# Kernel tuning notes

Measured on AMD Instinct MI355X. Metric: run time of the kernel, lower is better.

Reference implementation:

```python
import jax, jax.numpy as jnp
import numpy as np

B, S = 1, 1536
D_MODEL, NHEAD, HEAD_DIM = 1024, 16, 64
ROPE, NUM_SEQ = 32, 4
KVC, QC, D_FF = 256, 384, 4096
SPP = S // NUM_SEQ                      # seq per stock = 384
EPS_RMS = 1.1920929e-07                 # torch RMSNorm default eps = finfo(fp32).eps
ATTN_EPS = 1e-5
LAMBDA_INIT = 0.8 - 0.6 * float(np.exp(-0.3 * 0.0))  # depth 0 -> 0.2
SCALING = float(((HEAD_DIM + ROPE) // 2) ** -0.5)


def rmsnorm(x, w, eps=EPS_RMS):
    var = jnp.mean(jnp.square(x), axis=-1, keepdims=True)
    return x * jax.lax.rsqrt(var + eps) * w


def setup_inputs() -> dict:
    key = jax.random.key(0)
    ks = jax.random.split(key, 16)
    sd = 0.02
    inv_freq = 1.0 / (10000.0 ** (np.arange(0, ROPE // 4) / (ROPE // 4)))
    ang = np.arange(1, SPP)[:, None] * inv_freq[None, :]  # [SPP-1, ROPE//4]
    return {
        "x": jax.random.normal(ks[0], (B, S, D_MODEL), jnp.float32),
        "freqs_cos": jnp.asarray(np.cos(ang), jnp.float32),
        "freqs_sin": jnp.asarray(np.sin(ang), jnp.float32),
        "norm1_w": jnp.ones((D_MODEL,), jnp.float32),
        "norm2_w": jnp.ones((D_MODEL,), jnp.float32),
        "kv_down_w": jax.random.normal(ks[1], (KVC + ROPE, D_MODEL), jnp.float32) * sd,
        "q_down_w": jax.random.normal(ks[2], (QC, D_MODEL), jnp.float32) * sd,
        "kv_norm_w": jnp.ones((KVC,), jnp.float32),
        "q_norm_w": jnp.ones((QC,), jnp.float32),
        "kv_up_w": jax.random.normal(ks[3], (HEAD_DIM * NHEAD * 2, KVC), jnp.float32) * sd,
        "q_up_w": jax.random.normal(ks[4], ((HEAD_DIM + ROPE) * NHEAD, QC), jnp.float32) * sd,
        "lambda_q1": jax.random.normal(ks[5], (HEAD_DIM // 2,), jnp.float32) * 0.1,
        "lambda_k1": jax.random.normal(ks[6], (HEAD_DIM // 2,), jnp.float32) * 0.1,
        "lambda_q2": jax.random.normal(ks[7], (HEAD_DIM // 2,), jnp.float32) * 0.1,
        "lambda_k2": jax.random.normal(ks[8], (HEAD_DIM // 2,), jnp.float32) * 0.1,
        "attn_norm_w": jnp.ones((HEAD_DIM,), jnp.float32),
        "o_w": jax.random.normal(ks[9], (D_MODEL, NHEAD * HEAD_DIM), jnp.float32) * sd,
        "ff_in_w": jax.random.normal(ks[10], (D_FF * 2, D_MODEL), jnp.float32) * sd,
        "ff_out_w": jax.random.normal(ks[11], (D_MODEL, D_FF), jnp.float32) * sd,
    }


def reference(x, freqs_cos, freqs_sin, norm1_w, norm2_w, kv_down_w, q_down_w,
              kv_norm_w, q_norm_w, kv_up_w, q_up_w, lambda_q1, lambda_k1,
              lambda_q2, lambda_k2, attn_norm_w, o_w, ff_in_w, ff_out_w):
    b, s, _ = x.shape
    spp = s // NUM_SEQ
    H2, hd2 = 2 * NHEAD, HEAD_DIM // 2

    # block-tiled causal mask (1 = masked), matching mask.repeat(..., num_seq, num_seq)
    base = jnp.triu(jnp.ones((spp, spp), jnp.float32), 1)
    mask = jnp.tile(base, (NUM_SEQ, NUM_SEQ))  # [S, S]

    xin = rmsnorm(x, norm1_w)
    ckv = xin @ kv_down_w.T                                    # [B,S,KVC+ROPE]
    c_kv, k_rope = ckv[..., :KVC], ckv[..., KVC:]
    kv = (rmsnorm(c_kv, kv_norm_w) @ kv_up_w.T).reshape(b, s, NHEAD, 2 * HEAD_DIM)
    k, v = kv[..., :HEAD_DIM], kv[..., HEAD_DIM:]
    k = k.reshape(b, s, H2, hd2)
    qf = (rmsnorm(xin @ q_down_w.T, q_norm_w) @ q_up_w.T).reshape(b, s, NHEAD, HEAD_DIM + ROPE)
    q, q_rope = qf[..., :HEAD_DIM], qf[..., HEAD_DIM:]
    q = q.reshape(b, s, H2, hd2)
    k_rope = jnp.tile(k_rope[:, :, None, :], (1, 1, NHEAD, 1)).reshape(b, s, H2, ROPE // 2)
    q_rope = q_rope.reshape(b, s, H2, ROPE // 2)

    # rotary emb; position 0 of every ticker is left untouched (identity rotation)
    cos = jnp.concatenate([jnp.ones((1, ROPE // 4), freqs_cos.dtype), freqs_cos], 0)  # [spp, ROPE//4]
    sin = jnp.concatenate([jnp.zeros((1, ROPE // 4), freqs_sin.dtype), freqs_sin], 0)

    def rot(r):
        # S is laid out as (position, ticker) interleaved: s = p*NUM_SEQ + t
        r = r.reshape(b, spp, NUM_SEQ, H2, ROPE // 4, 2)
        c = cos[None, :, None, None, :]
        s_ = sin[None, :, None, None, :]
        r0, r1 = r[..., 0], r[..., 1]
        y = jnp.stack([r0 * c - r1 * s_, r0 * s_ + r1 * c], axis=-1)
        return y.reshape(b, s, H2, ROPE // 2)

    q = jnp.concatenate([q, rot(q_rope)], -1).transpose(0, 2, 1, 3)  # [B,2H,S,dk]
    k = jnp.concatenate([k, rot(k_rope)], -1).transpose(0, 2, 1, 3)
    v = v.transpose(0, 2, 1, 3)                                      # [B,H,S,hd]

    a = jnp.einsum('bhqd,bhkd->bhqk', q, k) * SCALING
    a = jnp.where(mask[None, None] == 1, -1e9, a)
    a = jax.nn.softmax(a, axis=-1)

    lam = jnp.exp(jnp.sum(lambda_k1 * lambda_q1)) - jnp.exp(jnp.sum(lambda_k2 * lambda_q2)) + LAMBDA_INIT
    a = a.reshape(b, NHEAD, 2, s, s)
    a1, a2 = a[:, :, 0], a[:, :, 1]
    g = jnp.mean(a1, axis=-2, keepdims=True)            # [B,H,1,S], broadcasts over queries
    a = a1 - lam * a2 + lam * g
    a = jnp.where(mask[None, None] == 1, 0.0, a)

    out = jnp.einsum('bhqk,bhkd->bhqd', a, v)           # [B,H,S,hd]
    out = rmsnorm(out.transpose(0, 2, 1, 3), attn_norm_w, eps=ATTN_EPS).transpose(0, 2, 1, 3)
    # faithful to source: raw reshape of [B,H,S,hd] -> [B,S,H*hd] (transposes cancel)
    out = out.reshape(b, s, NHEAD * HEAD_DIM)
    x = x + out @ o_w.T

    h = rmsnorm(x, norm2_w)
    uv = h @ ff_in_w.T
    u, vg = uv[..., :D_FF], uv[..., D_FF:]
    return x + (u * jax.nn.silu(vg)) @ ff_out_w.T
```

## Files before the change

kernel.cpp:

```cpp
#include <hip/hip_runtime.h>
#include <math.h>

#define S     1536
#define DM    1024
#define NH    16
#define H2N   32
#define HD    64
#define KVC   256
#define QC    384
#define DFF   4096
#define SPP   384
#define DQK   48
#define EPS_RMS  1.1920929e-07f
#define ATTN_EPS 1e-5f
#define SCALING  0.14433756729740643f

typedef float f32x4 __attribute__((ext_vector_type(4)));
typedef float f32x16 __attribute__((ext_vector_type(16)));
typedef short bf16x8 __attribute__((ext_vector_type(8)));

__device__ __forceinline__ short cvt_bf16(float f) {
  union { float f; unsigned u; } x; x.f = f;
  unsigned r = x.u + 0x7FFFu + ((x.u >> 16) & 1u);
  return (short)(r >> 16);
}
__device__ __forceinline__ unsigned pk2(float a, float b) {
  unsigned r;
  asm("v_cvt_pk_bf16_f32 %0, %1, %2" : "=v"(r) : "v"(a), "v"(b));
  return r;
}
__device__ __forceinline__ bf16x8 cvt8(float4 a, float4 b) {
  union { unsigned u[4]; bf16x8 v; } r;
  r.u[0] = pk2(a.x, a.y); r.u[1] = pk2(a.z, a.w);
  r.u[2] = pk2(b.x, b.y); r.u[3] = pk2(b.z, b.w);
  return r.v;
}

__global__ __launch_bounds__(256) void cvt_w4(const float* __restrict__ s0, int n0,
    const float* __restrict__ s1, int n1, const float* __restrict__ s2, int n2,
    const float* __restrict__ s3, int n3, short* __restrict__ dst) {
  long base = (long)blockIdx.x * 2048 + (long)threadIdx.x * 8;
  const float* src; long off;
  if (base < n0) { src = s0; off = base; }
  else if (base < (long)n0 + n1) { src = s1; off = base - n0; }
  else if (base < (long)n0 + n1 + n2) { src = s2; off = base - n0 - n1; }
  else { src = s3; off = base - n0 - n1 - n2; }
  float4 a = *reinterpret_cast<const float4*>(src + off);
  float4 b = *reinterpret_cast<const float4*>(src + off + 4);
  *reinterpret_cast<bf16x8*>(dst + base) = cvt8(a, b);
}

__global__ __launch_bounds__(256) void rmsnorm_bf(const float* __restrict__ in,
    const float* __restrict__ w, short* __restrict__ out,
    int cols, int ldin, int ldout, float eps) {
  const int row = blockIdx.x;
  const float* xr = in + (size_t)row * ldin;
  short* yr = out + (size_t)row * ldout;
  const int tid = threadIdx.x;
  float ss = 0.f;
  for (int c = tid << 2; c < cols; c += 1024) {
    float4 v = *reinterpret_cast<const float4*>(xr + c);
    ss += v.x*v.x + v.y*v.y + v.z*v.z + v.w*v.w;
  }
#pragma unroll
  for (int mm = 1; mm < 64; mm <<= 1) ss += __shfl_xor(ss, mm, 64);
  __shared__ float red[4];
  if ((tid & 63) == 0) red[tid >> 6] = ss;
  __syncthreads();
  float tot = red[0] + red[1] + red[2] + red[3];
  float scale = rsqrtf(tot / (float)cols + eps);
  for (int c = tid << 2; c < cols; c += 1024) {
    float4 v = *reinterpret_cast<const float4*>(xr + c);
    float4 wv = *reinterpret_cast<const float4*>(w + c);
    uint2 p;
    p.x = pk2(v.x*scale*wv.x, v.y*scale*wv.y);
    p.y = pk2(v.z*scale*wv.z, v.w*scale*wv.w);
    *reinterpret_cast<uint2*>(yr + c) = p;
  }
}

template<int ADD>
__global__ __launch_bounds__(256) void mgemm_nt(const short* __restrict__ A,
    const short* __restrict__ B, const float* __restrict__ src, float* __restrict__ C,
    int M, int N, int K, int lda, int ldb, int ldc) {
  __shared__ short As[64][72];
  __shared__ short Bs[64][72];
  const int bm = blockIdx.y * 64, bn = blockIdx.x * 64;
  const int tid = threadIdx.x;
  const int w = tid >> 6, lane = tid & 63;
  const int wr = (w >> 1) << 5, wc = (w & 1) << 5;
  const int srow = tid >> 2, sk = (tid & 3) << 4;
  const int lrow = lane & 15, lk8 = (lane >> 4) << 3;
  const int arow = bm + srow, brow = bn + srow;
  const bool bvalid = brow < N;
  f32x4 acc[2][2];
#pragma unroll
  for (int i = 0; i < 2; ++i)
#pragma unroll
    for (int j = 0; j < 2; ++j) acc[i][j] = (f32x4){0.f, 0.f, 0.f, 0.f};

  bf16x8 rah0, rah1, rbh0, rbh1;
  {
    const short* ap = A + (size_t)arow * lda + sk;
    rah0 = *reinterpret_cast<const bf16x8*>(ap);
    rah1 = *reinterpret_cast<const bf16x8*>(ap + 8);
  }
  rbh0 = (bf16x8){0,0,0,0,0,0,0,0}; rbh1 = rbh0;
  if (bvalid) {
    const short* bp = B + (size_t)brow * ldb + sk;
    rbh0 = *reinterpret_cast<const bf16x8*>(bp);
    rbh1 = *reinterpret_cast<const bf16x8*>(bp + 8);
  }

  for (int k0 = 0; k0 < K; k0 += 64) {
    bf16x8 va0 = rah0, va1 = rah1, vb0 = rbh0, vb1 = rbh1;
    __syncthreads();
    *reinterpret_cast<bf16x8*>(&As[srow][sk])     = va0;
    *reinterpret_cast<bf16x8*>(&As[srow][sk + 8]) = va1;
    *reinterpret_cast<bf16x8*>(&Bs[srow][sk])     = vb0;
    *reinterpret_cast<bf16x8*>(&Bs[srow][sk + 8]) = vb1;
    __syncthreads();
    const int kn = k0 + 64;
    if (kn < K) {
      const short* ap = A + (size_t)arow * lda + kn + sk;
      rah0 = *reinterpret_cast<const bf16x8*>(ap);
      rah1 = *reinterpret_cast<const bf16x8*>(ap + 8);
      if (bvalid) {
        const short* bp = B + (size_t)brow * ldb + kn + sk;
        rbh0 = *reinterpret_cast<const bf16x8*>(bp);
        rbh1 = *reinterpret_cast<const bf16x8*>(bp + 8);
      }
    }
#pragma unroll
    for (int kk = 0; kk < 2; ++kk) {
      bf16x8 af0 = *reinterpret_cast<bf16x8*>(&As[wr + lrow][(kk << 5) + lk8]);
      bf16x8 af1 = *reinterpret_cast<bf16x8*>(&As[wr + 16 + lrow][(kk << 5) + lk8]);
      bf16x8 bf0 = *reinterpret_cast<bf16x8*>(&Bs[wc + lrow][(kk << 5) + lk8]);
      bf16x8 bf1 = *reinterpret_cast<bf16x8*>(&Bs[wc + 16 + lrow][(kk << 5) + lk8]);
      acc[0][0] = __builtin_amdgcn_mfma_f32_16x16x32_bf16(af0, bf0, acc[0][0], 0, 0, 0);
      acc[0][1] = __builtin_amdgcn_mfma_f32_16x16x32_bf16(af0, bf1, acc[0][1], 0, 0, 0);
      acc[1][0] = __builtin_amdgcn_mfma_f32_16x16x32_bf16(af1, bf0, acc[1][0], 0, 0, 0);
      acc[1][1] = __builtin_amdgcn_mfma_f32_16x16x32_bf16(af1, bf1, acc[1][1], 0, 0, 0);
    }
  }
  const int crow0 = bm + wr + ((lane >> 4) << 2);
  const int ccol0 = bn + wc + lrow;
#pragma unroll
  for (int mi = 0; mi < 2; ++mi)
#pragma unroll
    for (int ni = 0; ni < 2; ++ni) {
      int colc = ccol0 + (ni << 4);
      if (colc < N) {
#pragma unroll
        for (int r = 0; r < 4; ++r) {
          int rowc = crow0 + (mi << 4) + r;
          float v = acc[mi][ni][r];
          if (ADD) v += src[(size_t)rowc * ldc + colc];
          C[(size_t)rowc * ldc + colc] = v;
        }
      }
    }
}

__global__ __launch_bounds__(256) void mgemm_glu(const short* __restrict__ A,
    const short* __restrict__ Bw, short* __restrict__ C,
    int M, int N, int K, int lda, int ldb, int ldc) {
  __shared__ short As[128][72];
  __shared__ short Bu[64][72];
  __shared__ short Bv[64][72];
  const int bm = blockIdx.y * 128, bn = blockIdx.x * 64;
  const int tid = threadIdx.x;
  const int w = tid >> 6, lane = tid & 63;
  const int wr = (w >> 1) << 6, wc = (w & 1) << 5;
  const int arow = bm + (tid >> 1), ac = (tid & 1) << 5;
  const int brow = bn + (tid >> 2), bc = (tid & 3) << 4;
  const int lrow = lane & 15, lk8 = (lane >> 4) << 3;
  f32x4 au[4][2], av[4][2];
#pragma unroll
  for (int i = 0; i < 4; ++i)
#pragma unroll
    for (int j = 0; j < 2; ++j) {
      au[i][j] = (f32x4){0.f, 0.f, 0.f, 0.f};
      av[i][j] = (f32x4){0.f, 0.f, 0.f, 0.f};
    }
  bf16x8 ra[4], ru[2], rv[2];
  {
    const short* ap = A + (size_t)arow * lda + ac;
    const short* up = Bw + (size_t)brow * ldb + bc;
    const short* vp = Bw + (size_t)(N + brow) * ldb + bc;
#pragma unroll
    for (int e = 0; e < 4; ++e) ra[e] = *reinterpret_cast<const bf16x8*>(ap + (e << 3));
    ru[0] = *reinterpret_cast<const bf16x8*>(up);
    ru[1] = *reinterpret_cast<const bf16x8*>(up + 8);
    rv[0] = *reinterpret_cast<const bf16x8*>(vp);
    rv[1] = *reinterpret_cast<const bf16x8*>(vp + 8);
  }
  for (int k0 = 0; k0 < K; k0 += 64) {
    __syncthreads();
#pragma unroll
    for (int e = 0; e < 4; ++e)
      *reinterpret_cast<bf16x8*>(&As[tid >> 1][ac + (e << 3)]) = ra[e];
    *reinterpret_cast<bf16x8*>(&Bu[tid >> 2][bc])     = ru[0];
    *reinterpret_cast<bf16x8*>(&Bu[tid >> 2][bc + 8]) = ru[1];
    *reinterpret_cast<bf16x8*>(&Bv[tid >> 2][bc])     = rv[0];
    *reinterpret_cast<bf16x8*>(&Bv[tid >> 2][bc + 8]) = rv[1];
    __syncthreads();
    const int kn = k0 + 64;
    if (kn < K) {
      const short* ap = A + (size_t)arow * lda + kn + ac;
      const short* up = Bw + (size_t)brow * ldb + kn + bc;
      const short* vp = Bw + (size_t)(N + brow) * ldb + kn + bc;
#pragma unroll
      for (int e = 0; e < 4; ++e) ra[e] = *reinterpret_cast<const bf16x8*>(ap + (e << 3));
      ru[0] = *reinterpret_cast<const bf16x8*>(up);
      ru[1] = *reinterpret_cast<const bf16x8*>(up + 8);
      rv[0] = *reinterpret_cast<const bf16x8*>(vp);
      rv[1] = *reinterpret_cast<const bf16x8*>(vp + 8);
    }
#pragma unroll
    for (int kk = 0; kk < 2; ++kk) {
      bf16x8 af[4], uf[2], vf[2];
#pragma unroll
      for (int i = 0; i < 4; ++i)
        af[i] = *reinterpret_cast<bf16x8*>(&As[wr + (i << 4) + lrow][(kk << 5) + lk8]);
#pragma unroll
      for (int j = 0; j < 2; ++j) {
        uf[j] = *reinterpret_cast<bf16x8*>(&Bu[wc + (j << 4) + lrow][(kk << 5) + lk8]);
        vf[j] = *reinterpret_cast<bf16x8*>(&Bv[wc + (j << 4) + lrow][(kk << 5) + lk8]);
      }
#pragma unroll
      for (int i = 0; i < 4; ++i)
#pragma unroll
        for (int j = 0; j < 2; ++j) {
          au[i][j] = __builtin_amdgcn_mfma_f32_16x16x32_bf16(af[i], uf[j], au[i][j], 0, 0, 0);
          av[i][j] = __builtin_amdgcn_mfma_f32_16x16x32_bf16(af[i], vf[j], av[i][j], 0, 0, 0);
        }
    }
  }
  const int crow0 = bm + wr + ((lane >> 4) << 2);
  const int ccol0 = bn + wc + lrow;
#pragma unroll
  for (int mi = 0; mi < 4; ++mi)
#pragma unroll
    for (int ni = 0; ni < 2; ++ni) {
      int colc = ccol0 + (ni << 4);
#pragma unroll
      for (int r = 0; r < 4; ++r) {
        int rowc = crow0 + (mi << 4) + r;
        float uu = au[mi][ni][r], vg = av[mi][ni][r];
        float sig = 1.0f / (1.0f + __expf(-vg));
        C[(size_t)rowc * ldc + colc] = cvt_bf16(uu * vg * sig);
      }
    }
}

__global__ __launch_bounds__(256) void build_qk(const float* __restrict__ qf,
    const float* __restrict__ kvb, const float* __restrict__ ckv,
    const float* __restrict__ fc, const float* __restrict__ fs,
    short* __restrict__ Qb, short* __restrict__ Kb) {
  int t = blockIdx.x * 256 + threadIdx.x;
  int h2 = blockIdx.y;
  if (t >= S) return;
  int hh = h2 >> 1, par = h2 & 1;
  const float* qrow = qf + (size_t)t*1536 + hh*96;
  const float* krow = kvb + (size_t)t*2048 + hh*128;
  unsigned qu[24], ku[24];
#pragma unroll
  for (int xq = 0; xq < 8; ++xq) {
    float4 qv = *reinterpret_cast<const float4*>(qrow + par*32 + (xq<<2));
    float4 kv = *reinterpret_cast<const float4*>(krow + par*32 + (xq<<2));
    qu[xq*2]   = pk2(qv.x, qv.y); qu[xq*2+1] = pk2(qv.z, qv.w);
    ku[xq*2]   = pk2(kv.x, kv.y); ku[xq*2+1] = pk2(kv.z, kv.w);
  }
  int p = t >> 2;
  const float* qr = qrow + 64 + par*16;
  const float* kr = ckv + (size_t)t*288 + 256 + par*16;
#pragma unroll
  for (int mq = 0; mq < 8; ++mq) {
    float c = 1.f, sn = 0.f;
    if (p > 0) { c = fc[(p-1)*8 + mq]; sn = fs[(p-1)*8 + mq]; }
    float q0 = qr[2*mq], q1 = qr[2*mq+1];
    qu[16 + mq] = pk2(q0*c - q1*sn, q0*sn + q1*c);
    float k0 = kr[2*mq], k1 = kr[2*mq+1];
    ku[16 + mq] = pk2(k0*c - k1*sn, k0*sn + k1*c);
  }
  unsigned* qo = (unsigned*)(Qb + ((size_t)h2*S + t)*DQK);
  unsigned* ko = (unsigned*)(Kb + ((size_t)h2*S + t)*DQK);
#pragma unroll
  for (int e = 0; e < 6; ++e) {
    *reinterpret_cast<uint4*>(qo + (e<<2)) = make_uint4(qu[e*4], qu[e*4+1], qu[e*4+2], qu[e*4+3]);
    *reinterpret_cast<uint4*>(ko + (e<<2)) = make_uint4(ku[e*4], ku[e*4+1], ku[e*4+2], ku[e*4+3]);
  }
}

__global__ __launch_bounds__(256) void vt_build(const float* __restrict__ kvb,
    short* __restrict__ Vt) {
  const int hh = blockIdx.x;
  const int t0 = blockIdx.y << 7;
  __shared__ short Ts[128][74];
  const int tl = threadIdx.x >> 3, dp = (threadIdx.x & 7) << 3;
#pragma unroll
  for (int pass = 0; pass < 4; ++pass) {
    int t = t0 + (pass << 5) + tl;
    const float* vp = kvb + (size_t)t*2048 + hh*128 + 64 + dp;
    float4 a = *reinterpret_cast<const float4*>(vp);
    float4 b = *reinterpret_cast<const float4*>(vp + 4);
    *reinterpret_cast<bf16x8*>(&Ts[(pass << 5) + tl][dp]) = cvt8(a, b);
  }
  __syncthreads();
  for (int idx = threadIdx.x; idx < 1024; idx += 256) {
    int d = idx >> 4, tseg = (idx & 15) << 3;
    bf16x8 v;
#pragma unroll
    for (int e = 0; e < 8; ++e) v[e] = Ts[tseg + e][d];
    *reinterpret_cast<bf16x8*>(Vt + ((size_t)hh*HD + d)*S + t0 + tseg) = v;
  }
}

__global__ void compute_lam(const float* __restrict__ lq1, const float* __restrict__ lk1,
                            const float* __restrict__ lq2, const float* __restrict__ lk2,
                            float* __restrict__ lamp) {
  int t = threadIdx.x;
  float a = lq1[t]*lk1[t];
  float b = lq2[t]*lk2[t];
#pragma unroll
  for (int mm = 1; mm < 32; mm <<= 1) { a += __shfl_xor(a, mm, 32); b += __shfl_xor(b, mm, 32); }
  if (t == 0) lamp[0] = expf(a) - expf(b) + 0.2f;
}

__global__ __launch_bounds__(256) void flash_mfma(const short* __restrict__ Qb,
    const short* __restrict__ Kb, const short* __restrict__ Vg,
    float* __restrict__ Ob, float* __restrict__ rowm, float* __restrict__ rowl,
    float* __restrict__ Ob1a, float* __restrict__ Ob1b,
    float* __restrict__ rm1, float* __restrict__ rl1) {
  const int h2 = blockIdx.y;
  const int hh = h2 >> 1;
  const int z  = blockIdx.z;
  const int tid = threadIdx.x;
  const int w = tid >> 6, lane = tid & 63;
  const int ql = lane & 31, h = lane >> 5;
  const int cq = blockIdx.x / 3, k = blockIdx.x % 3;
  const int qi = k + 3*w;
  const int qbase = cq*SPP + (qi << 5);
  const int ri0w = qi << 5;

  __shared__ __align__(16) float Ot[4][32][36];

  bf16x8 qf0, qf1, qf2;
  {
    const short* qp = Qb + ((size_t)h2*S + qbase + ql)*DQK + (h << 3);
    qf0 = *reinterpret_cast<const bf16x8*>(qp);
    qf1 = *reinterpret_cast<const bf16x8*>(qp + 16);
    qf2 = *reinterpret_cast<const bf16x8*>(qp + 32);
  }
  const short* Kbase = Kb + (size_t)h2*S*DQK + (h << 3);
  const short* V0 = Vg + ((size_t)hh*HD + ql)*S + (h << 3);
  const short* V1 = Vg + ((size_t)hh*HD + 32 + ql)*S + (h << 3);

  float m = -1e30f, l = 0.f;
  f32x16 o0, o1;
#pragma unroll
  for (int r = 0; r < 16; ++r) { o0[r] = 0.f; o1[r] = 0.f; }

  for (int c = (z << 1); c < (z << 1) + 2; ++c) {
    for (int jr = 0; jr <= ri0w; jr += 32) {
      const int j0 = c*SPP + jr;
      const bool diag = (jr == ri0w);
      const short* kp = Kbase + (size_t)(j0 + ql)*DQK;
      bf16x8 kf0 = *reinterpret_cast<const bf16x8*>(kp);
      bf16x8 kf1 = *reinterpret_cast<const bf16x8*>(kp + 16);
      bf16x8 kf2 = *reinterpret_cast<const bf16x8*>(kp + 32);
      bf16x8 v00 = *reinterpret_cast<const bf16x8*>(V0 + j0);
      bf16x8 v01 = *reinterpret_cast<const bf16x8*>(V0 + j0 + 16);
      bf16x8 v10 = *reinterpret_cast<const bf16x8*>(V1 + j0);
      bf16x8 v11 = *reinterpret_cast<const bf16x8*>(V1 + j0 + 16);

      f32x16 st;
#pragma unroll
      for (int r = 0; r < 16; ++r) st[r] = 0.f;
      st = __builtin_amdgcn_mfma_f32_32x32x16_bf16(kf0, qf0, st, 0, 0, 0);
      st = __builtin_amdgcn_mfma_f32_32x32x16_bf16(kf1, qf1, st, 0, 0, 0);
      st = __builtin_amdgcn_mfma_f32_32x32x16_bf16(kf2, qf2, st, 0, 0, 0);

      if (diag) {
#pragma unroll
        for (int r = 0; r < 16; ++r) {
          int kl = (r & 3) + ((r >> 2) << 3) + (h << 2);
          st[r] = (kl <= ql) ? st[r] * SCALING : -1e30f;
        }
      } else {
#pragma unroll
        for (int r = 0; r < 16; ++r) st[r] *= SCALING;
      }

      float tm = st[0];
#pragma unroll
      for (int r = 1; r < 16; ++r) tm = fmaxf(tm, st[r]);
      tm = fmaxf(tm, __shfl_xor(tm, 32));
      if (__any(tm > m + 8.0f)) {
        float mnew = fmaxf(m, tm);
        float sc = __expf(m - mnew);
        m = mnew;
        l *= sc;
#pragma unroll
        for (int r = 0; r < 16; ++r) { o0[r] *= sc; o1[r] *= sc; }
      }
      float ps = 0.f;
#pragma unroll
      for (int r = 0; r < 16; ++r) { float p = __expf(st[r] - m); st[r] = p; ps += p; }
      ps += __shfl_xor(ps, 32);
      l += ps;

      unsigned A0 = pk2(st[0],  st[1]),  B0 = pk2(st[2],  st[3]);
      unsigned C0 = pk2(st[4],  st[5]),  D0 = pk2(st[6],  st[7]);
      unsigned A1 = pk2(st[8],  st[9]),  B1 = pk2(st[10], st[11]);
      unsigned C1 = pk2(st[12], st[13]), D1 = pk2(st[14], st[15]);
      unsigned xA0 = (unsigned)__shfl_xor((int)A0, 32), xB0 = (unsigned)__shfl_xor((int)B0, 32);
      unsigned xC0 = (unsigned)__shfl_xor((int)C0, 32), xD0 = (unsigned)__shfl_xor((int)D0, 32);
      unsigned xA1 = (unsigned)__shfl_xor((int)A1, 32), xB1 = (unsigned)__shfl_xor((int)B1, 32);
      unsigned xC1 = (unsigned)__shfl_xor((int)C1, 32), xD1 = (unsigned)__shfl_xor((int)D1, 32);
      union { unsigned u[4]; bf16x8 v; } P0, P1;
      P0.u[0] = h ? xC0 : A0;  P0.u[1] = h ? xD0 : B0;
      P0.u[2] = h ? C0 : xA0;  P0.u[3] = h ? D0 : xB0;
      P1.u[0] = h ? xC1 : A1;  P1.u[1] = h ? xD1 : B1;
      P1.u[2] = h ? C1 : xA1;  P1.u[3] = h ? D1 : xB1;

      o0 = __builtin_amdgcn_mfma_f32_32x32x16_bf16(v00, P0.v, o0, 0, 0, 0);
      o0 = __builtin_amdgcn_mfma_f32_32x32x16_bf16(v01, P1.v, o0, 0, 0, 0);
      o1 = __builtin_amdgcn_mfma_f32_32x32x16_bf16(v10, P0.v, o1, 0, 0, 0);
      o1 = __builtin_amdgcn_mfma_f32_32x32x16_bf16(v11, P1.v, o1, 0, 0, 0);
    }
  }

  float* ot = &Ot[w][0][0];
  float* orow;
  if (z == 0) orow = Ob + ((size_t)h2*S + qbase)*HD;
  else orow = (h2 < 16) ? Ob1a + ((size_t)h2*S + qbase)*HD
                        : Ob1b + ((size_t)(h2 - 16)*S + qbase)*HD;
#pragma unroll
  for (int r = 0; r < 16; ++r) {
    int dl = (r & 3) + ((r >> 2) << 3) + (h << 2);
    ot[ql*36 + dl] = o0[r];
  }
#pragma unroll
  for (int it = 0; it < 4; ++it) {
    int idx = lane + (it << 6);
    int row = idx >> 3, c4 = (idx & 7) << 2;
    float4 v = *reinterpret_cast<float4*>(&ot[row*36 + c4]);
    *reinterpret_cast<float4*>(&orow[(size_t)row*HD + c4]) = v;
  }
#pragma unroll
  for (int r = 0; r < 16; ++r) {
    int dl = (r & 3) + ((r >> 2) << 3) + (h << 2);
    ot[ql*36 + dl] = o1[r];
  }
#pragma unroll
  for (int it = 0; it < 4; ++it) {
    int idx = lane + (it << 6);
    int row = idx >> 3, c4 = (idx & 7) << 2;
    float4 v = *reinterpret_cast<float4*>(&ot[row*36 + c4]);
    *reinterpret_cast<float4*>(&orow[(size_t)row*HD + 32 + c4]) = v;
  }
  if (lane < 32) {
    if (z == 0) { rowm[h2*S + qbase + lane] = m; rowl[h2*S + qbase + lane] = l; }
    else        { rm1[h2*S + qbase + lane] = m;  rl1[h2*S + qbase + lane] = l; }
  }
}

__global__ __launch_bounds__(256) void merge_flash(float* __restrict__ Ob,
    float* __restrict__ rowm, float* __restrict__ rowl,
    const float* __restrict__ Ob1a, const float* __restrict__ Ob1b,
    const float* __restrict__ rm1, const float* __restrict__ rl1) {
  const int gid = blockIdx.x * 4 + (threadIdx.x >> 6);
  const int d = threadIdx.x & 63;
  const int h2 = gid / S;
  float m0 = rowm[gid], l0 = rowl[gid], m1 = rm1[gid], l1 = rl1[gid];
  float m = fmaxf(m0, m1);
  float w0 = __expf(m0 - m), w1 = __expf(m1 - m);
  float linv = 1.0f / (l0*w0 + l1*w1);
  const float* o1 = (h2 < 16) ? (Ob1a + (size_t)gid*HD)
                              : (Ob1b + ((size_t)gid - (size_t)16*S)*HD);
  float v0 = Ob[(size_t)gid*HD + d];
  float v1 = o1[d];
  Ob[(size_t)gid*HD + d] = (v0*w0 + v1*w1) * linv;
  if (d == 0) { rowm[gid] = m; rowl[gid] = l0*w0 + l1*w1; }
}

__global__ __launch_bounds__(256) void colsum_mfma(const short* __restrict__ Qb,
    const short* __restrict__ Kb, const float* __restrict__ rowm,
    const float* __restrict__ rowl, float* __restrict__ gcol) {
  const int jt = blockIdx.x;
  const int hh = blockIdx.y, h2 = hh << 1;
  const int cK = jt / 12, jr32 = jt % 12;
  const int jr = jr32 << 5;
  const int j0 = cK*SPP + jr;
  const int tid = threadIdx.x;
  const int w = tid >> 6, lane = tid & 63;
  const int ql = lane & 31, h = lane >> 5;

  bf16x8 kf0, kf1, kf2;
  {
    const short* kp = Kb + ((size_t)h2*S + j0 + ql)*DQK + (h << 3);
    kf0 = *reinterpret_cast<const bf16x8*>(kp);
    kf1 = *reinterpret_cast<const bf16x8*>(kp + 16);
    kf2 = *reinterpret_cast<const bf16x8*>(kp + 32);
  }
  const int nt = 12 - jr32;
  const int T = nt << 2;
  float gs[16];
#pragma unroll
  for (int r = 0; r < 16; ++r) gs[r] = 0.f;

  for (int tt = w; tt < T; tt += 4) {
    int cq = tt / nt, qrem = tt - cq*nt;
    int qi = jr32 + qrem;
    int i0 = cq*SPP + (qi << 5);
    const bool diag = (qrem == 0);
    const short* qp = Qb + ((size_t)h2*S + i0 + ql)*DQK + (h << 3);
    bf16x8 qf0 = *reinterpret_cast<const bf16x8*>(qp);
    bf16x8 qf1 = *reinterpret_cast<const bf16x8*>(qp + 16);
    bf16x8 qf2 = *reinterpret_cast<const bf16x8*>(qp + 32);
    f32x16 st;
#pragma unroll
    for (int r = 0; r < 16; ++r) st[r] = 0.f;
    st = __builtin_amdgcn_mfma_f32_32x32x16_bf16(kf0, qf0, st, 0, 0, 0);
    st = __builtin_amdgcn_mfma_f32_32x32x16_bf16(kf1, qf1, st, 0, 0, 0);
    st = __builtin_amdgcn_mfma_f32_32x32x16_bf16(kf2, qf2, st, 0, 0, 0);
    float Mq = rowm[h2*S + i0 + ql];
    float Lq = 1.0f / rowl[h2*S + i0 + ql];
    if (diag) {
#pragma unroll
      for (int r = 0; r < 16; ++r) {
        int kl = (r & 3) + ((r >> 2) << 3) + (h << 2);
        if (kl <= ql) gs[r] += __expf(st[r]*SCALING - Mq) * Lq;
      }
    } else {
#pragma unroll
      for (int r = 0; r < 16; ++r) gs[r] += __expf(st[r]*SCALING - Mq) * Lq;
    }
  }
  __shared__ float gw[4][32];
#pragma unroll
  for (int r = 0; r < 16; ++r) {
    float v = gs[r];
#pragma unroll
    for (int mm = 1; mm < 32; mm <<= 1) v += __shfl_xor(v, mm, 32);
    if (ql == 0) gw[w][(r & 3) + ((r >> 2) << 3) + (h << 2)] = v;
  }
  __syncthreads();
  if (tid < 32) {
    float s = gw[0][tid] + gw[1][tid] + gw[2][tid] + gw[3][tid];
    gcol[hh*S + j0 + tid] = s * (1.0f / (float)S);
  }
}

__global__ __launch_bounds__(256) void build_wpre(const float* __restrict__ gcol,
    const float* __restrict__ kvb, float* __restrict__ Wpre) {
  const int hh = blockIdx.x >> 2;
  const int dq = (blockIdx.x & 3) << 4;
  __shared__ float Wt[SPP][16];
  const int tid = threadIdx.x;
  for (int idx = tid; idx < SPP*16; idx += 256) {
    int r = idx >> 4, dd = idx & 15;
    float val = 0.f;
#pragma unroll
    for (int b2 = 0; b2 < 4; ++b2) {
      int j = b2*SPP + r;
      val = fmaf(gcol[hh*S + j], kvb[(size_t)j*2048 + hh*128 + 64 + dq + dd], val);
    }
    Wt[r][dd] = val;
  }
  __syncthreads();
  if (tid < 16) {
    float run = 0.f;
    for (int r = 0; r < SPP; ++r) { run += Wt[r][tid]; Wt[r][tid] = run; }
  }
  __syncthreads();
  for (int idx = tid; idx < SPP*16; idx += 256) {
    int r = idx >> 4, dd = idx & 15;
    Wpre[((size_t)hh*SPP + r)*HD + dq + dd] = Wt[r][dd];
  }
}

__global__ __launch_bounds__(64) void combine_rms(const float* __restrict__ Ob,
    const float* __restrict__ Wpre, const float* __restrict__ lamp,
    const float* __restrict__ anw, short* __restrict__ attno) {
  const int t = blockIdx.x, h = blockIdx.y, d = threadIdx.x;
  const float lam = lamp[0];
  const float o1 = Ob[((size_t)(2*h)*S + t)*HD + d];
  const float o2 = Ob[((size_t)(2*h+1)*S + t)*HD + d];
  const float w3 = Wpre[((size_t)h*SPP + (t % SPP))*HD + d];
  float val = o1 - lam*o2 + lam*w3;
  float ss = val*val;
#pragma unroll
  for (int mm = 1; mm < 64; mm <<= 1) ss += __shfl_xor(ss, mm, 64);
  float scale = rsqrtf(ss * (1.0f/HD) + ATTN_EPS) * anw[d];
  int tn = h*96 + (t >> 4);
  int cn = ((t & 15) << 6) + d;
  attno[(size_t)tn*DM + cn] = cvt_bf16(val * scale);
}

extern "C" void kernel_launch(void* const* d_in, const int* in_sizes, int n_in,
                              void* d_out, int out_size, void* d_ws, size_t ws_size,
                              hipStream_t stream) {
  (void)in_sizes; (void)n_in; (void)out_size;
  const float* x    = (const float*)d_in[0];
  const float* fc   = (const float*)d_in[1];
  const float* fs   = (const float*)d_in[2];
  const float* n1w  = (const float*)d_in[3];
  const float* n2w  = (const float*)d_in[4];
  const float* kvdw = (const float*)d_in[5];
  const float* qdw  = (const float*)d_in[6];
  const float* kvnw = (const float*)d_in[7];
  const float* qnw  = (const float*)d_in[8];
  const float* kvuw = (const float*)d_in[9];
  const float* quw  = (const float*)d_in[10];
  const float* lq1  = (const float*)d_in[11];
  const float* lk1  = (const float*)d_in[12];
  const float* lq2  = (const float*)d_in[13];
  const float* lk2  = (const float*)d_in[14];
  const float* anw  = (const float*)d_in[15];
  const float* ow   = (const float*)d_in[16];
  const float* ffiw = (const float*)d_in[17];
  const float* ffow = (const float*)d_in[18];
  float* out = (float*)d_out;
  float* ws  = (float*)d_ws;

  float* xin   = ws;
  float* ckv   = xin   + (size_t)S*DM;
  float* qmid  = ckv   + (size_t)S*288;
  float* kvb   = qmid  + (size_t)S*QC;
  float* qf    = kvb   + (size_t)S*2048;
  float* Qb    = qf    + (size_t)S*1536;
  float* Kb    = Qb    + (size_t)H2N*S*DQK;
  float* Obuf  = Kb    + (size_t)H2N*S*DQK;
  float* rowm  = Obuf  + (size_t)H2N*S*HD;
  float* rowl  = rowm  + (size_t)H2N*S;
  float* gcol  = rowl  + (size_t)H2N*S;
  float* Wpre  = gcol  + (size_t)NH*S;
  float* attno = Wpre  + (size_t)NH*SPP*HD;
  float* lamp  = attno + (size_t)S*DM;
  short* fbufs = (short*)kvb;
  float* Ob1a = xin;
  float* Ob1b = qf;
  float* rm1  = qf + (size_t)16*S*HD;
  float* rl1  = rm1 + (size_t)H2N*S;
  short* Qb_bf = (short*)Qb;
  short* Kb_bf = (short*)Kb;
  short* Vt_bf = (short*)Qb + 2359296;
  short* xin_bf  = (short*)xin;
  short* ckv_bf  = (short*)Obuf;
  short* qmid_bf = ckv_bf + (size_t)S*KVC;
  short* h_bf    = (short*)xin;
  short* attno_bf = (short*)attno;
  short* kvdw_bf = (short*)attno;
  short* qdw_bf  = kvdw_bf + 294912;
  short* kvuw_bf = qdw_bf  + 393216;
  short* quw_bf  = kvuw_bf + 524288;
  short* ffiw_bf = (short*)Qb;
  short* ow_bf   = ffiw_bf + 8388608;
  short* ffow_bf = (short*)Obuf;
  if (ws_size < (size_t)18063376 * sizeof(float)) return;

  cvt_w4<<<880, 256, 0, stream>>>(kvdw, 294912, qdw, 393216, kvuw, 524288, quw, 589824, kvdw_bf);
  rmsnorm_bf<<<S, 256, 0, stream>>>(x, n1w, xin_bf, DM, DM, DM, EPS_RMS);
  { dim3 g(5, 24);  mgemm_nt<0><<<g, 256, 0, stream>>>(xin_bf, kvdw_bf, nullptr, ckv, S, 288, DM, DM, DM, 288); }
  { dim3 g(6, 24);  mgemm_nt<0><<<g, 256, 0, stream>>>(xin_bf, qdw_bf,  nullptr, qmid, S, QC, DM, DM, DM, QC); }
  rmsnorm_bf<<<S, 256, 0, stream>>>(ckv,  kvnw, ckv_bf,  KVC, 288, KVC, EPS_RMS);
  rmsnorm_bf<<<S, 256, 0, stream>>>(qmid, qnw,  qmid_bf, QC,  QC,  QC,  EPS_RMS);
  { dim3 g(32, 24); mgemm_nt<0><<<g, 256, 0, stream>>>(ckv_bf,  kvuw_bf, nullptr, kvb, S, 2048, KVC, KVC, KVC, 2048); }
  { dim3 g(24, 24); mgemm_nt<0><<<g, 256, 0, stream>>>(qmid_bf, quw_bf,  nullptr, qf,  S, 1536, QC,  QC,  QC,  1536); }
  { dim3 g(6, 32);  build_qk<<<g, 256, 0, stream>>>(qf, kvb, ckv, fc, fs, Qb_bf, Kb_bf); }
  { dim3 g(16, 12); vt_build<<<g, 256, 0, stream>>>(kvb, Vt_bf); }
  compute_lam<<<1, 32, 0, stream>>>(lq1, lk1, lq2, lk2, lamp);
  { dim3 g(12, 32, 2); flash_mfma<<<g, 256, 0, stream>>>(Qb_bf, Kb_bf, Vt_bf, Obuf, rowm, rowl,
                                                         Ob1a, Ob1b, rm1, rl1); }
  merge_flash<<<(H2N*S)/4, 256, 0, stream>>>(Obuf, rowm, rowl, Ob1a, Ob1b, rm1, rl1);
  { dim3 g(48, 16); colsum_mfma<<<g, 256, 0, stream>>>(Qb_bf, Kb_bf, rowm, rowl, gcol); }
  cvt_w4<<<4608, 256, 0, stream>>>(ffiw, 8388608, ow, 1048576, nullptr, 0, nullptr, 0, ffiw_bf);
  build_wpre<<<64, 256, 0, stream>>>(gcol, kvb, Wpre);
  { dim3 g(S, 16);  combine_rms<<<g, 64, 0, stream>>>(Obuf, Wpre, lamp, anw, attno_bf); }
  cvt_w4<<<2048, 256, 0, stream>>>(ffow, 4194304, nullptr, 0, nullptr, 0, nullptr, 0, ffow_bf);
  { dim3 g(16, 24); mgemm_nt<1><<<g, 256, 0, stream>>>(attno_bf, ow_bf, x, out, S, DM, DM, DM, DM, DM); }
  rmsnorm_bf<<<S, 256, 0, stream>>>(out, n2w, h_bf, DM, DM, DM, EPS_RMS);
  { dim3 g(64, 12); mgemm_glu<<<g, 256, 0, stream>>>(h_bf, ffiw_bf, fbufs, S, DFF, DM, DM, DM, DFF); }
  { dim3 g(16, 24); mgemm_nt<1><<<g, 256, 0, stream>>>(fbufs, ffow_bf, out, out, S, DM, DFF, DFF, DFF, DM); }
}
```

Before: 243.8 us.

## Split-K the output and FFN-down GEMMs and fuse residual sum into RMSNorm

The o-projection and FFN-down GEMMs now use a two-way split-K kernel that writes two partial buffers. This doubles the grid from 384 to 768 blocks to fill the GPU better. A new fused kernel adds the two partials and the residual, writes x, and computes RMSNorm into bf16 in one pass, replacing the separate residual add and norm. A small fadd2 kernel then reduces the FFN-down partials into the output. The cost is extra fp32 partial-buffer traffic and one extra launch.

```diff
diff --git a/kernel.cpp b/kernel.cpp
--- a/kernel.cpp
+++ b/kernel.cpp
@@ -77,6 +77,43 @@
     p.y = pk2(v.z*scale*wv.z, v.w*scale*wv.w);
     *reinterpret_cast<uint2*>(yr + c) = p;
   }
+}
+
+__global__ __launch_bounds__(256) void rmsnorm_sum_bf(const float* __restrict__ p0,
+    const float* __restrict__ p1, const float* __restrict__ xres,
+    const float* __restrict__ w, float* __restrict__ outw, short* __restrict__ yb,
+    float eps) {
+  const int row = blockIdx.x;
+  const int c = threadIdx.x << 2;
+  const size_t base = (size_t)row * DM + c;
+  float4 a = *reinterpret_cast<const float4*>(p0 + base);
+  float4 b = *reinterpret_cast<const float4*>(p1 + base);
+  float4 xv = *reinterpret_cast<const float4*>(xres + base);
+  float4 v = make_float4(a.x+b.x+xv.x, a.y+b.y+xv.y, a.z+b.z+xv.z, a.w+b.w+xv.w);
+  *reinterpret_cast<float4*>(outw + base) = v;
+  float ss = v.x*v.x + v.y*v.y + v.z*v.z + v.w*v.w;
+#pragma unroll
+  for (int mm = 1; mm < 64; mm <<= 1) ss += __shfl_xor(ss, mm, 64);
+  __shared__ float red[4];
+  if ((threadIdx.x & 63) == 0) red[threadIdx.x >> 6] = ss;
+  __syncthreads();
+  float tot = red[0] + red[1] + red[2] + red[3];
+  float scale = rsqrtf(tot * (1.0f / (float)DM) + eps);
+  float4 wv = *reinterpret_cast<const float4*>(w + c);
+  uint2 p;
+  p.x = pk2(v.x*scale*wv.x, v.y*scale*wv.y);
+  p.y = pk2(v.z*scale*wv.z, v.w*scale*wv.w);
+  *reinterpret_cast<uint2*>(yb + base) = p;
+}
+
+__global__ __launch_bounds__(256) void fadd2(float* __restrict__ out,
+    const float* __restrict__ p0, const float* __restrict__ p1) {
+  size_t i = ((size_t)blockIdx.x * 256 + threadIdx.x) << 2;
+  float4 o = *reinterpret_cast<float4*>(out + i);
+  float4 a = *reinterpret_cast<const float4*>(p0 + i);
+  float4 b = *reinterpret_cast<const float4*>(p1 + i);
+  o.x += a.x + b.x; o.y += a.y + b.y; o.z += a.z + b.z; o.w += a.w + b.w;
+  *reinterpret_cast<float4*>(out + i) = o;
 }
 
 template<int ADD>
@@ -158,6 +195,80 @@
           if (ADD) v += src[(size_t)rowc * ldc + colc];
           C[(size_t)rowc * ldc + colc] = v;
         }
+      }
+    }
+}
+
+__global__ __launch_bounds__(256) void mgemm_sk(const short* __restrict__ A,
+    const short* __restrict__ B, float* __restrict__ P0, float* __restrict__ P1,
+    int M, int N, int K2, int lda, int ldb, int ldc) {
+  __shared__ short As[64][72];
+  __shared__ short Bs[64][72];
+  const int bm = blockIdx.y * 64, bn = blockIdx.x * 64;
+  const int koff = blockIdx.z * K2;
+  float* C = blockIdx.z ? P1 : P0;
+  const int tid = threadIdx.x;
+  const int w = tid >> 6, lane = tid & 63;
+  const int wr = (w >> 1) << 5, wc = (w & 1) << 5;
+  const int srow = tid >> 2, sk = (tid & 3) << 4;
+  const int lrow = lane & 15, lk8 = (lane >> 4) << 3;
+  const int arow = bm + srow, brow = bn + srow;
+  f32x4 acc[2][2];
+#pragma unroll
+  for (int i = 0; i < 2; ++i)
+#pragma unroll
+    for (int j = 0; j < 2; ++j) acc[i][j] = (f32x4){0.f, 0.f, 0.f, 0.f};
+
+  bf16x8 rah0, rah1, rbh0, rbh1;
+  {
+    const short* ap = A + (size_t)arow * lda + koff + sk;
+    rah0 = *reinterpret_cast<const bf16x8*>(ap);
+    rah1 = *reinterpret_cast<const bf16x8*>(ap + 8);
+    const short* bp = B + (size_t)brow * ldb + koff + sk;
+    rbh0 = *reinterpret_cast<const bf16x8*>(bp);
+    rbh1 = *reinterpret_cast<const bf16x8*>(bp + 8);
+  }
+  const int kend = koff + K2;
+  for (int k0 = koff; k0 < kend; k0 += 64) {
+    bf16x8 va0 = rah0, va1 = rah1, vb0 = rbh0, vb1 = rbh1;
+    __syncthreads();
+    *reinterpret_cast<bf16x8*>(&As[srow][sk])     = va0;
+    *reinterpret_cast<bf16x8*>(&As[srow][sk + 8]) = va1;
+    *reinterpret_cast<bf16x8*>(&Bs[srow][sk])     = vb0;
+    *reinterpret_cast<bf16x8*>(&Bs[srow][sk + 8]) = vb1;
+    __syncthreads();
+    const int kn = k0 + 64;
+    if (kn < kend) {
+      const short* ap = A + (size_t)arow * lda + kn + sk;
+      rah0 = *reinterpret_cast<const bf16x8*>(ap);
+      rah1 = *reinterpret_cast<const bf16x8*>(ap + 8);
+      const short* bp = B + (size_t)brow * ldb + kn + sk;
+      rbh0 = *reinterpret_cast<const bf16x8*>(bp);
+      rbh1 = *reinterpret_cast<const bf16x8*>(bp + 8);
+    }
+#pragma unroll
+    for (int kk = 0; kk < 2; ++kk) {
+      bf16x8 af0 = *reinterpret_cast<bf16x8*>(&As[wr + lrow][(kk << 5) + lk8]);
+      bf16x8 af1 = *reinterpret_cast<bf16x8*>(&As[wr + 16 + lrow][(kk << 5) + lk8]);
+      bf16x8 bf0 = *reinterpret_cast<bf16x8*>(&Bs[wc + lrow][(kk << 5) + lk8]);
+      bf16x8 bf1 = *reinterpret_cast<bf16x8*>(&Bs[wc + 16 + lrow][(kk << 5) + lk8]);
+      acc[0][0] = __builtin_amdgcn_mfma_f32_16x16x32_bf16(af0, bf0, acc[0][0], 0, 0, 0);
+      acc[0][1] = __builtin_amdgcn_mfma_f32_16x16x32_bf16(af0, bf1, acc[0][1], 0, 0, 0);
+      acc[1][0] = __builtin_amdgcn_mfma_f32_16x16x32_bf16(af1, bf0, acc[1][0], 0, 0, 0);
+      acc[1][1] = __builtin_amdgcn_mfma_f32_16x16x32_bf16(af1, bf1, acc[1][1], 0, 0, 0);
+    }
+  }
+  const int crow0 = bm + wr + ((lane >> 4) << 2);
+  const int ccol0 = bn + wc + lrow;
+#pragma unroll
+  for (int mi = 0; mi < 2; ++mi)
+#pragma unroll
+    for (int ni = 0; ni < 2; ++ni) {
+      int colc = ccol0 + (ni << 4);
+#pragma unroll
+      for (int r = 0; r < 4; ++r) {
+        int rowc = crow0 + (mi << 4) + r;
+        C[(size_t)rowc * ldc + colc] = acc[mi][ni][r];
       }
     }
 }
@@ -651,7 +762,7 @@
   short* xin_bf  = (short*)xin;
   short* ckv_bf  = (short*)Obuf;
   short* qmid_bf = ckv_bf + (size_t)S*KVC;
-  short* h_bf    = (short*)xin;
+  short* h_bf    = (short*)ckv;
   short* attno_bf = (short*)attno;
   short* kvdw_bf = (short*)attno;
   short* qdw_bf  = kvdw_bf + 294912;
@@ -660,6 +771,8 @@
   short* ffiw_bf = (short*)Qb;
   short* ow_bf   = ffiw_bf + 8388608;
   short* ffow_bf = (short*)Obuf;
+  float* psum0 = xin;
+  float* psum1 = qf;
   if (ws_size < (size_t)18063376 * sizeof(float)) return;
 
   cvt_w4<<<880, 256, 0, stream>>>(kvdw, 294912, qdw, 393216, kvuw, 524288, quw, 589824, kvdw_bf);
@@ -681,8 +794,9 @@
   build_wpre<<<64, 256, 0, stream>>>(gcol, kvb, Wpre);
   { dim3 g(S, 16);  combine_rms<<<g, 64, 0, stream>>>(Obuf, Wpre, lamp, anw, attno_bf); }
   cvt_w4<<<2048, 256, 0, stream>>>(ffow, 4194304, nullptr, 0, nullptr, 0, nullptr, 0, ffow_bf);
-  { dim3 g(16, 24); mgemm_nt<1><<<g, 256, 0, stream>>>(attno_bf, ow_bf, x, out, S, DM, DM, DM, DM, DM); }
-  rmsnorm_bf<<<S, 256, 0, stream>>>(out, n2w, h_bf, DM, DM, DM, EPS_RMS);
+  { dim3 g(16, 24, 2); mgemm_sk<<<g, 256, 0, stream>>>(attno_bf, ow_bf, psum0, psum1, S, DM, 512, DM, DM, DM); }
+  rmsnorm_sum_bf<<<S, 256, 0, stream>>>(psum0, psum1, x, n2w, out, h_bf, EPS_RMS);
   { dim3 g(64, 12); mgemm_glu<<<g, 256, 0, stream>>>(h_bf, ffiw_bf, fbufs, S, DFF, DM, DM, DM, DFF); }
-  { dim3 g(16, 24); mgemm_nt<1><<<g, 256, 0, stream>>>(fbufs, ffow_bf, out, out, S, DM, DFF, DFF, DFF, DM); }
-}
+  { dim3 g(16, 24, 2); mgemm_sk<<<g, 256, 0, stream>>>(fbufs, ffow_bf, psum0, psum1, S, DM, 2048, DFF, DFF, DM); }
+  fadd2<<<1536, 256, 0, stream>>>(out, psum0, psum1);
+}
```

Result: faster. 235.9 us (-3.2%).
